# Kernel optimization log

Hardware: AMD Instinct MI355X
Metric: run time of the kernel (lower is better)

## Reference

```python
import jax, jax.numpy as jnp
import numpy as np

N_EMBED = 16384
EMBED_DIM = 256
BETA = 1.0  # default forward arg


def setup_inputs() -> dict:
    key = jax.random.key(0)
    k1, k2 = jax.random.split(key)
    z = jax.random.normal(k1, (8, EMBED_DIM, 32, 32), dtype=jnp.float32)
    # nn.Embedding init: uniform(-1/n_embed, 1/n_embed)
    embed_w = jax.random.uniform(k2, (N_EMBED, EMBED_DIM), dtype=jnp.float32,
                                 minval=-1.0 / N_EMBED, maxval=1.0 / N_EMBED)
    return {"z": z, "embed_w": embed_w}


def reference(z, embed_w):
    B, C, H, W = z.shape
    zb = jnp.transpose(z, (0, 2, 3, 1))            # (B,H,W,C)
    zf = zb.reshape(B * H * W, C)                  # (BHW, C)
    # squared L2 distances to every code: ||z||^2 + ||e||^2 - 2 z.e
    d = (jnp.sum(zf ** 2, axis=1, keepdims=True)
         + jnp.sum(embed_w ** 2, axis=1)
         - 2.0 * jnp.einsum('bd,nd->bn', zf, embed_w))  # (BHW, n_embed)
    idx = jnp.argmin(d, axis=1)                    # (BHW,)
    z_q = embed_w[idx].reshape(B, H, W, C)         # codebook gather
    loss = (BETA * jnp.mean((jax.lax.stop_gradient(z_q) - zb) ** 2)
            + jnp.mean((z_q - jax.lax.stop_gradient(zb)) ** 2))
    # straight-through estimator
    z_q = zb + jax.lax.stop_gradient(z_q - zb)
    z_q = jnp.transpose(z_q, (0, 3, 1, 2))         # (B,C,H,W)
    return z_q, loss
```

## Files before the change

kernel.cpp:

```cpp
#include <hip/hip_runtime.h>
#include <hip/hip_bf16.h>
#include <stdint.h>


typedef __attribute__((ext_vector_type(8))) short bf16x8;
typedef __attribute__((ext_vector_type(8))) unsigned short ushort8v;
typedef __attribute__((ext_vector_type(4))) float f32x4;

__device__ __forceinline__ unsigned short f2bf(float f) {
  unsigned u = __float_as_uint(f);
  return (unsigned short)((u + 0x7FFFu + ((u >> 16) & 1u)) >> 16);
}

typedef const __attribute__((address_space(1))) unsigned char* gas1;
typedef __attribute__((address_space(3))) unsigned char* las3;
__device__ __forceinline__ void cp16(const void* g, void* l) {
  __builtin_amdgcn_global_load_lds((gas1)g, (las3)l, 16, 0, 0);
}

__global__ void k_prep_z(const float* __restrict__ z, unsigned short* __restrict__ zp) {
  __shared__ float tile[32][129];
  int bid = blockIdx.x;
  int b = bid >> 6, ct = (bid >> 3) & 7, hwt = bid & 7;
  int t = threadIdx.x;
  const float* src = z + b * 262144 + ct * 32 * 1024 + hwt * 128;
#pragma unroll
  for (int it = 0; it < 16; ++it) {
    int e = it * 256 + t;
    int cl = e >> 7, hl = e & 127;
    tile[cl][hl] = src[cl * 1024 + hl];
  }
  __syncthreads();
  int mt = b * 8 + hwt;
  unsigned short* dst = zp + mt * 32768 + ct * 4096;
#pragma unroll
  for (int it = 0; it < 2; ++it) {
    int cell = it * 256 + t;
    int kg = cell >> 7, r = cell & 127;
    ushort8v v;
#pragma unroll
    for (int j = 0; j < 8; ++j) v[j] = f2bf(tile[kg * 8 + j][r]);
    *(ushort8v*)(dst + cell * 8) = v;
  }
}

__global__ void k_prep_e(const float* __restrict__ ew, unsigned short* __restrict__ ep,
                         float* __restrict__ h2) {
  int t = threadIdx.x;
  int n = blockIdx.x * 32 + (t >> 3);
  int nb = n >> 7, col = n & 127;
  float s = 0.0f;
#pragma unroll
  for (int it = 0; it < 4; ++it) {
    int cellk = (t & 7) + it * 8;
    const float4 x = *(const float4*)(ew + n * 256 + cellk * 8);
    const float4 y = *(const float4*)(ew + n * 256 + cellk * 8 + 4);
    s += x.x * x.x + x.y * x.y + x.z * x.z + x.w * x.w
       + y.x * y.x + y.y * y.y + y.z * y.z + y.w * y.w;
    int ks = cellk >> 2, kg = cellk & 3;
    ushort8v v;
    v[0] = f2bf(x.x); v[1] = f2bf(x.y); v[2] = f2bf(x.z); v[3] = f2bf(x.w);
    v[4] = f2bf(y.x); v[5] = f2bf(y.y); v[6] = f2bf(y.z); v[7] = f2bf(y.w);
    *(ushort8v*)(ep + nb * 32768 + ks * 4096 + kg * 1024 + col * 8) = v;
  }
#pragma unroll
  for (int off = 1; off <= 4; off <<= 1) s += __shfl_xor(s, off);
  if ((t & 7) == 0) h2[n] = 0.5f * s;
}

__global__ __launch_bounds__(256, 2) void k_main(
    const unsigned short* __restrict__ zp, const unsigned short* __restrict__ ep,
    const float* __restrict__ h2, int2* __restrict__ partial) {
  __shared__ unsigned char bLds[2][8192];
  int seg = blockIdx.x;
  int mt = blockIdx.y;
  int t = threadIdx.x, wv = t >> 6, lane = t & 63;
  int l15 = lane & 15, kg = lane >> 4;

  bf16x8 av[16];
  const unsigned short* abase = zp + mt * 32768;
#pragma unroll
  for (int m = 0; m < 2; ++m)
#pragma unroll
    for (int ks = 0; ks < 8; ++ks)
      av[m * 8 + ks] = *(const bf16x8*)(abase + ks * 4096 + kg * 1024 +
                                        (wv * 32 + m * 16 + l15) * 8);

  const unsigned char* bsrc = (const unsigned char*)ep + seg * 1048576;
  const float* hseg = h2 + seg * 2048;

#pragma unroll
  for (int i = 0; i < 2; ++i)
    cp16(bsrc + i * 4096 + wv * 1024 + lane * 16, &bLds[0][i * 4096 + wv * 1024]);

  float hv[8];
#pragma unroll
  for (int nf = 0; nf < 8; ++nf) hv[nf] = hseg[nf * 16 + l15];

  f32x4 acc[2][8];
#pragma unroll
  for (int m = 0; m < 2; ++m)
#pragma unroll
    for (int nf = 0; nf < 8; ++nf)
      acc[m][nf] = (f32x4){-hv[nf], -hv[nf], -hv[nf], -hv[nf]};

  float best[2][4];
#pragma unroll
  for (int m = 0; m < 2; ++m)
#pragma unroll
    for (int r = 0; r < 4; ++r) best[m][r] = -3.4e38f;

  __syncthreads();

  for (int ch = 0; ch < 16; ++ch) {
    float hn[8];
    if (ch < 15) {
#pragma unroll
      for (int nf = 0; nf < 8; ++nf) hn[nf] = hseg[(ch + 1) * 128 + nf * 16 + l15];
    }
#pragma unroll
    for (int ks = 0; ks < 8; ++ks) {
      int g = ch * 8 + ks;
      int cur = g & 1;
      if (g < 127) {
#pragma unroll
        for (int i = 0; i < 2; ++i)
          cp16(bsrc + (g + 1) * 8192 + i * 4096 + wv * 1024 + lane * 16,
               &bLds[cur ^ 1][i * 4096 + wv * 1024]);
      }
      bf16x8 bv[8];
#pragma unroll
      for (int nf = 0; nf < 8; ++nf)
        bv[nf] = *(const bf16x8*)(&bLds[cur][kg * 2048 + (nf * 16 + l15) * 16]);
#pragma unroll
      for (int m = 0; m < 2; ++m)
#pragma unroll
        for (int nf = 0; nf < 8; ++nf)
          acc[m][nf] = __builtin_amdgcn_mfma_f32_16x16x32_bf16(
              av[m * 8 + ks], bv[nf], acc[m][nf], 0, 0, 0);
      __syncthreads();
    }
    int colbase = ch * 128 + l15;
#pragma unroll
    for (int m = 0; m < 2; ++m)
#pragma unroll
      for (int nf = 0; nf < 8; ++nf) {
        unsigned lcol = (unsigned)(colbase + nf * 16);
#pragma unroll
        for (int r = 0; r < 4; ++r) {
          unsigned p = (__float_as_uint(acc[m][nf][r]) & 0xFFFFF800u) | lcol;
          best[m][r] = fmaxf(best[m][r], __uint_as_float(p));
        }
      }
    if (ch < 15) {
#pragma unroll
      for (int m = 0; m < 2; ++m)
#pragma unroll
        for (int nf = 0; nf < 8; ++nf)
          acc[m][nf] = (f32x4){-hn[nf], -hn[nf], -hn[nf], -hn[nf]};
    }
  }

#pragma unroll
  for (int m = 0; m < 2; ++m)
#pragma unroll
    for (int r = 0; r < 4; ++r) {
      float bvv = best[m][r];
#pragma unroll
      for (int off = 1; off <= 8; off <<= 1) bvv = fmaxf(bvv, __shfl_xor(bvv, off));
      if (l15 == 0) {
        unsigned bits = __float_as_uint(bvv);
        int gidx = seg * 2048 + (int)(bits & 0x7FFu);
        int row = mt * 128 + wv * 32 + m * 16 + kg * 4 + r;
        partial[seg * 8192 + row] = make_int2((int)bits, gidx);
      }
    }
}

__global__ void k_rg(const int2* __restrict__ partial, const float* __restrict__ ew,
                     float* __restrict__ rows) {
  int row = blockIdx.x * 4 + (threadIdx.x >> 6);
  int lane = threadIdx.x & 63;
  float bb = -3.4e38f;
  int bi = 0;
#pragma unroll
  for (int s = 0; s < 8; ++s) {
    int2 p = partial[s * 8192 + row];
    float v = __int_as_float(p.x);
    if (v > bb) { bb = v; bi = p.y; }
  }
  float4 v = *(const float4*)(ew + bi * 256 + lane * 4);
  *(float4*)(rows + row * 256 + lane * 4) = v;
}

__global__ void k_out(const float* __restrict__ rows, const float* __restrict__ z,
                      float* __restrict__ out) {
  __shared__ float tile[32][132];
  int bid = blockIdx.x;
  int b = bid >> 6, hwt = (bid >> 3) & 7, ct = bid & 7;
  int t = threadIdx.x;
  int hw0 = hwt * 128, c0 = ct * 32;
  const float* rbase = rows + (b * 1024 + hw0) * 256 + c0;
#pragma unroll
  for (int it = 0; it < 4; ++it) {
    int p = it * 32 + (t >> 3);
    int c = (t & 7) * 4;
    float4 v = *(const float4*)(rbase + p * 256 + c);
    tile[c][p] = v.x; tile[c + 1][p] = v.y; tile[c + 2][p] = v.z; tile[c + 3][p] = v.w;
  }
  __syncthreads();
  float ls = 0.0f;
  int obase = b * 262144 + c0 * 1024 + hw0;
#pragma unroll
  for (int it = 0; it < 4; ++it) {
    int c = it * 8 + (t >> 5);
    int p = (t & 31) * 4;
    float4 q = *(const float4*)(&tile[c][p]);
    float4 zv = *(const float4*)(z + obase + c * 1024 + p);
    float dx = q.x - zv.x, dy = q.y - zv.y, dz = q.z - zv.z, dw = q.w - zv.w;
    ls += dx * dx + dy * dy + dz * dz + dw * dw;
    *(float4*)(out + obase + c * 1024 + p) = q;
  }
#pragma unroll
  for (int off = 32; off; off >>= 1) ls += __shfl_xor(ls, off);
  if ((t & 63) == 0) atomicAdd(out + 2097152, ls * (2.0f / 2097152.0f));
}

extern "C" void kernel_launch(void* const* d_in, const int* in_sizes, int n_in,
                              void* d_out, int out_size, void* d_ws, size_t ws_size,
                              hipStream_t stream) {
  const float* z = (const float*)d_in[0];
  const float* ew = (const float*)d_in[1];
  float* out = (float*)d_out;
  unsigned char* ws = (unsigned char*)d_ws;
  unsigned short* zp = (unsigned short*)ws;
  unsigned short* ep = (unsigned short*)(ws + (4u << 20));
  float* h2 = (float*)(ws + (12u << 20));
  int2* partial = (int2*)(ws + (12u << 20) + 65536);
  float* rows = (float*)(ws + (13u << 20));

  k_prep_z<<<512, 256, 0, stream>>>(z, zp);
  k_prep_e<<<512, 256, 0, stream>>>(ew, ep, h2);
  k_main<<<dim3(8, 64), 256, 0, stream>>>(zp, ep, h2, partial);
  k_rg<<<2048, 256, 0, stream>>>(partial, ew, rows);
  hipMemsetAsync(out + 2097152, 0, 4, stream);
  k_out<<<512, 256, 0, stream>>>(rows, z, out);
}
```

Measured before the change: 180.7 us.

## Fuse prep and finalize kernels, double main grid segments, use larger k-stages

The z and codebook prep kernels are merged into one launch that also zeroes the loss slot, replacing the memset. The reduce-gather and output-transpose kernels are merged, so the intermediate gathered-rows buffer is no longer written and reread. The main kernel splits the codebook into 16 segments instead of 8 to launch more blocks, and stages 16KB of B per barrier instead of 8KB, halving the barrier count. It also raises launch bounds to 3 blocks per CU and wraps the MFMA section in s_setprio. In exchange, the finalize step reads twice as many partials and each main block uses more LDS.

```diff
diff --git a/kernel.cpp b/kernel.cpp
--- a/kernel.cpp
+++ b/kernel.cpp
@@ -18,60 +18,62 @@
   __builtin_amdgcn_global_load_lds((gas1)g, (las3)l, 16, 0, 0);
 }
 
-__global__ void k_prep_z(const float* __restrict__ z, unsigned short* __restrict__ zp) {
-  __shared__ float tile[32][129];
+__global__ void k_prep(const float* __restrict__ z, const float* __restrict__ ew,
+                       unsigned short* __restrict__ zp, unsigned short* __restrict__ ep,
+                       float* __restrict__ h2, float* __restrict__ out) {
+  __shared__ float tile[32][132];
   int bid = blockIdx.x;
-  int b = bid >> 6, ct = (bid >> 3) & 7, hwt = bid & 7;
   int t = threadIdx.x;
-  const float* src = z + b * 262144 + ct * 32 * 1024 + hwt * 128;
-#pragma unroll
-  for (int it = 0; it < 16; ++it) {
-    int e = it * 256 + t;
-    int cl = e >> 7, hl = e & 127;
-    tile[cl][hl] = src[cl * 1024 + hl];
-  }
-  __syncthreads();
-  int mt = b * 8 + hwt;
-  unsigned short* dst = zp + mt * 32768 + ct * 4096;
-#pragma unroll
-  for (int it = 0; it < 2; ++it) {
-    int cell = it * 256 + t;
-    int kg = cell >> 7, r = cell & 127;
-    ushort8v v;
-#pragma unroll
-    for (int j = 0; j < 8; ++j) v[j] = f2bf(tile[kg * 8 + j][r]);
-    *(ushort8v*)(dst + cell * 8) = v;
-  }
-}
-
-__global__ void k_prep_e(const float* __restrict__ ew, unsigned short* __restrict__ ep,
-                         float* __restrict__ h2) {
-  int t = threadIdx.x;
-  int n = blockIdx.x * 32 + (t >> 3);
-  int nb = n >> 7, col = n & 127;
-  float s = 0.0f;
-#pragma unroll
-  for (int it = 0; it < 4; ++it) {
-    int cellk = (t & 7) + it * 8;
-    const float4 x = *(const float4*)(ew + n * 256 + cellk * 8);
-    const float4 y = *(const float4*)(ew + n * 256 + cellk * 8 + 4);
-    s += x.x * x.x + x.y * x.y + x.z * x.z + x.w * x.w
-       + y.x * y.x + y.y * y.y + y.z * y.z + y.w * y.w;
-    int ks = cellk >> 2, kg = cellk & 3;
-    ushort8v v;
-    v[0] = f2bf(x.x); v[1] = f2bf(x.y); v[2] = f2bf(x.z); v[3] = f2bf(x.w);
-    v[4] = f2bf(y.x); v[5] = f2bf(y.y); v[6] = f2bf(y.z); v[7] = f2bf(y.w);
-    *(ushort8v*)(ep + nb * 32768 + ks * 4096 + kg * 1024 + col * 8) = v;
-  }
-#pragma unroll
-  for (int off = 1; off <= 4; off <<= 1) s += __shfl_xor(s, off);
-  if ((t & 7) == 0) h2[n] = 0.5f * s;
-}
-
-__global__ __launch_bounds__(256, 2) void k_main(
+  if (bid < 512) {
+    int b = bid >> 6, ct = (bid >> 3) & 7, hwt = bid & 7;
+    const float* src = z + b * 262144 + ct * 32768 + hwt * 128;
+#pragma unroll
+    for (int it = 0; it < 4; ++it) {
+      int cell = it * 1024 + t * 4;
+      int cl = cell >> 7, hl = cell & 127;
+      float4 v = *(const float4*)(src + cl * 1024 + hl);
+      *(float4*)(&tile[cl][hl]) = v;
+    }
+    __syncthreads();
+    int mt = b * 8 + hwt;
+    unsigned short* dst = zp + mt * 32768 + ct * 4096;
+#pragma unroll
+    for (int it = 0; it < 2; ++it) {
+      int cell = it * 256 + t;
+      int kg = cell >> 7, r = cell & 127;
+      ushort8v v;
+#pragma unroll
+      for (int j = 0; j < 8; ++j) v[j] = f2bf(tile[kg * 8 + j][r]);
+      *(ushort8v*)(dst + cell * 8) = v;
+    }
+  } else {
+    if (bid == 512 && t == 0) out[2097152] = 0.0f;
+    int n = (bid - 512) * 32 + (t >> 3);
+    int nb = n >> 7, col = n & 127;
+    float s = 0.0f;
+#pragma unroll
+    for (int it = 0; it < 4; ++it) {
+      int cellk = (t & 7) + it * 8;
+      const float4 x = *(const float4*)(ew + n * 256 + cellk * 8);
+      const float4 y = *(const float4*)(ew + n * 256 + cellk * 8 + 4);
+      s += x.x * x.x + x.y * x.y + x.z * x.z + x.w * x.w
+         + y.x * y.x + y.y * y.y + y.z * y.z + y.w * y.w;
+      int ks = cellk >> 2, kg = cellk & 3;
+      ushort8v v;
+      v[0] = f2bf(x.x); v[1] = f2bf(x.y); v[2] = f2bf(x.z); v[3] = f2bf(x.w);
+      v[4] = f2bf(y.x); v[5] = f2bf(y.y); v[6] = f2bf(y.z); v[7] = f2bf(y.w);
+      *(ushort8v*)(ep + nb * 32768 + ks * 4096 + kg * 1024 + col * 8) = v;
+    }
+#pragma unroll
+    for (int off = 1; off <= 4; off <<= 1) s += __shfl_xor(s, off);
+    if ((t & 7) == 0) h2[n] = 0.5f * s;
+  }
+}
+
+__global__ __launch_bounds__(256, 3) void k_main(
     const unsigned short* __restrict__ zp, const unsigned short* __restrict__ ep,
     const float* __restrict__ h2, int2* __restrict__ partial) {
-  __shared__ unsigned char bLds[2][8192];
+  __shared__ unsigned char bLds[2][16384];
   int seg = blockIdx.x;
   int mt = blockIdx.y;
   int t = threadIdx.x, wv = t >> 6, lane = t & 63;
@@ -86,79 +88,70 @@
       av[m * 8 + ks] = *(const bf16x8*)(abase + ks * 4096 + kg * 1024 +
                                         (wv * 32 + m * 16 + l15) * 8);
 
-  const unsigned char* bsrc = (const unsigned char*)ep + seg * 1048576;
-  const float* hseg = h2 + seg * 2048;
-
-#pragma unroll
-  for (int i = 0; i < 2; ++i)
+  const unsigned char* bsrc = (const unsigned char*)ep + seg * 524288;
+  const float* hseg = h2 + seg * 1024;
+
+#pragma unroll
+  for (int i = 0; i < 4; ++i)
     cp16(bsrc + i * 4096 + wv * 1024 + lane * 16, &bLds[0][i * 4096 + wv * 1024]);
 
-  float hv[8];
-#pragma unroll
-  for (int nf = 0; nf < 8; ++nf) hv[nf] = hseg[nf * 16 + l15];
-
   f32x4 acc[2][8];
+  float best[2][4];
 #pragma unroll
   for (int m = 0; m < 2; ++m)
 #pragma unroll
-    for (int nf = 0; nf < 8; ++nf)
-      acc[m][nf] = (f32x4){-hv[nf], -hv[nf], -hv[nf], -hv[nf]};
-
-  float best[2][4];
-#pragma unroll
-  for (int m = 0; m < 2; ++m)
-#pragma unroll
     for (int r = 0; r < 4; ++r) best[m][r] = -3.4e38f;
 
   __syncthreads();
 
-  for (int ch = 0; ch < 16; ++ch) {
-    float hn[8];
-    if (ch < 15) {
-#pragma unroll
-      for (int nf = 0; nf < 8; ++nf) hn[nf] = hseg[(ch + 1) * 128 + nf * 16 + l15];
-    }
-#pragma unroll
-    for (int ks = 0; ks < 8; ++ks) {
-      int g = ch * 8 + ks;
-      int cur = g & 1;
-      if (g < 127) {
-#pragma unroll
-        for (int i = 0; i < 2; ++i)
-          cp16(bsrc + (g + 1) * 8192 + i * 4096 + wv * 1024 + lane * 16,
-               &bLds[cur ^ 1][i * 4096 + wv * 1024]);
+#pragma unroll 4
+  for (int s = 0; s < 32; ++s) {
+    int cur = s & 1;
+    if (s < 31) {
+#pragma unroll
+      for (int i = 0; i < 4; ++i)
+        cp16(bsrc + (s + 1) * 16384 + i * 4096 + wv * 1024 + lane * 16,
+             &bLds[cur ^ 1][i * 4096 + wv * 1024]);
+    }
+    int nb = s >> 2, ph = s & 3;
+    if (ph == 0) {
+#pragma unroll
+      for (int nf = 0; nf < 8; ++nf) {
+        float h = hseg[nb * 128 + nf * 16 + l15];
+        acc[0][nf] = (f32x4){-h, -h, -h, -h};
+        acc[1][nf] = acc[0][nf];
       }
+    }
+    __builtin_amdgcn_s_setprio(1);
+#pragma unroll
+    for (int k2 = 0; k2 < 2; ++k2) {
       bf16x8 bv[8];
 #pragma unroll
       for (int nf = 0; nf < 8; ++nf)
-        bv[nf] = *(const bf16x8*)(&bLds[cur][kg * 2048 + (nf * 16 + l15) * 16]);
+        bv[nf] = *(const bf16x8*)(&bLds[cur][k2 * 8192 + kg * 2048 + (nf * 16 + l15) * 16]);
 #pragma unroll
       for (int m = 0; m < 2; ++m)
 #pragma unroll
         for (int nf = 0; nf < 8; ++nf)
           acc[m][nf] = __builtin_amdgcn_mfma_f32_16x16x32_bf16(
-              av[m * 8 + ks], bv[nf], acc[m][nf], 0, 0, 0);
-      __syncthreads();
-    }
-    int colbase = ch * 128 + l15;
-#pragma unroll
-    for (int m = 0; m < 2; ++m)
-#pragma unroll
-      for (int nf = 0; nf < 8; ++nf) {
-        unsigned lcol = (unsigned)(colbase + nf * 16);
-#pragma unroll
-        for (int r = 0; r < 4; ++r) {
-          unsigned p = (__float_as_uint(acc[m][nf][r]) & 0xFFFFF800u) | lcol;
-          best[m][r] = fmaxf(best[m][r], __uint_as_float(p));
+              av[m * 8 + ph * 2 + k2], bv[nf], acc[m][nf], 0, 0, 0);
+    }
+    __builtin_amdgcn_s_setprio(0);
+    if (ph == 3) {
+      int colbase = nb * 128 + l15;
+#pragma unroll
+      for (int m = 0; m < 2; ++m)
+#pragma unroll
+        for (int nf = 0; nf < 8; ++nf) {
+          unsigned lcol = (unsigned)(colbase + nf * 16);
+#pragma unroll
+          for (int r = 0; r < 4; ++r) {
+            unsigned p = (__float_as_uint(acc[m][nf][r]) & 0xFFFFF800u) | lcol;
+            best[m][r] = fmaxf(best[m][r], __uint_as_float(p));
+          }
         }
-      }
-    if (ch < 15) {
-#pragma unroll
-      for (int m = 0; m < 2; ++m)
-#pragma unroll
-        for (int nf = 0; nf < 8; ++nf)
-          acc[m][nf] = (f32x4){-hn[nf], -hn[nf], -hn[nf], -hn[nf]};
-    }
+    }
+    __syncthreads();
   }
 
 #pragma unroll
@@ -170,47 +163,48 @@
       for (int off = 1; off <= 8; off <<= 1) bvv = fmaxf(bvv, __shfl_xor(bvv, off));
       if (l15 == 0) {
         unsigned bits = __float_as_uint(bvv);
-        int gidx = seg * 2048 + (int)(bits & 0x7FFu);
+        int gidx = seg * 1024 + (int)(bits & 0x7FFu);
         int row = mt * 128 + wv * 32 + m * 16 + kg * 4 + r;
         partial[seg * 8192 + row] = make_int2((int)bits, gidx);
       }
     }
 }
 
-__global__ void k_rg(const int2* __restrict__ partial, const float* __restrict__ ew,
-                     float* __restrict__ rows) {
-  int row = blockIdx.x * 4 + (threadIdx.x >> 6);
-  int lane = threadIdx.x & 63;
-  float bb = -3.4e38f;
-  int bi = 0;
-#pragma unroll
-  for (int s = 0; s < 8; ++s) {
-    int2 p = partial[s * 8192 + row];
-    float v = __int_as_float(p.x);
-    if (v > bb) { bb = v; bi = p.y; }
-  }
-  float4 v = *(const float4*)(ew + bi * 256 + lane * 4);
-  *(float4*)(rows + row * 256 + lane * 4) = v;
-}
-
-__global__ void k_out(const float* __restrict__ rows, const float* __restrict__ z,
-                      float* __restrict__ out) {
+__global__ void k_fin(const int2* __restrict__ partial, const float* __restrict__ ew,
+                      const float* __restrict__ z, float* __restrict__ out) {
   __shared__ float tile[32][132];
+  __shared__ int codeIdx[128];
   int bid = blockIdx.x;
   int b = bid >> 6, hwt = (bid >> 3) & 7, ct = bid & 7;
   int t = threadIdx.x;
-  int hw0 = hwt * 128, c0 = ct * 32;
-  const float* rbase = rows + (b * 1024 + hw0) * 256 + c0;
-#pragma unroll
-  for (int it = 0; it < 4; ++it) {
-    int p = it * 32 + (t >> 3);
-    int c = (t & 7) * 4;
-    float4 v = *(const float4*)(rbase + p * 256 + c);
-    tile[c][p] = v.x; tile[c + 1][p] = v.y; tile[c + 2][p] = v.z; tile[c + 3][p] = v.w;
+  int rowbase = b * 1024 + hwt * 128;
+  if (t < 128) {
+    int row = rowbase + t;
+    float bb = -3.4e38f;
+    int bi = 0;
+#pragma unroll
+    for (int s = 0; s < 16; ++s) {
+      int2 p = partial[s * 8192 + row];
+      float v = __int_as_float(p.x);
+      if (v > bb) { bb = v; bi = p.y; }
+    }
+    codeIdx[t] = bi;
+  }
+  __syncthreads();
+  int c0 = ct * 32;
+  {
+    int p = t >> 1, half = t & 1;
+    const float* er = ew + codeIdx[p] * 256 + c0 + half * 16;
+#pragma unroll
+    for (int j = 0; j < 4; ++j) {
+      float4 v = *(const float4*)(er + j * 4);
+      int c = half * 16 + j * 4;
+      tile[c][p] = v.x; tile[c + 1][p] = v.y; tile[c + 2][p] = v.z; tile[c + 3][p] = v.w;
+    }
   }
   __syncthreads();
   float ls = 0.0f;
-  int obase = b * 262144 + c0 * 1024 + hw0;
+  int obase = b * 262144 + c0 * 1024 + hwt * 128;
 #pragma unroll
   for (int it = 0; it < 4; ++it) {
     int c = it * 8 + (t >> 5);
@@ -237,12 +231,8 @@
   unsigned short* ep = (unsigned short*)(ws + (4u << 20));
   float* h2 = (float*)(ws + (12u << 20));
   int2* partial = (int2*)(ws + (12u << 20) + 65536);
-  float* rows = (float*)(ws + (13u << 20));
-
-  k_prep_z<<<512, 256, 0, stream>>>(z, zp);
-  k_prep_e<<<512, 256, 0, stream>>>(ew, ep, h2);
-  k_main<<<dim3(8, 64), 256, 0, stream>>>(zp, ep, h2, partial);
-  k_rg<<<2048, 256, 0, stream>>>(partial, ew, rows);
-  hipMemsetAsync(out + 2097152, 0, 4, stream);
-  k_out<<<512, 256, 0, stream>>>(rows, z, out);
-}
+
+  k_prep<<<1024, 256, 0, stream>>>(z, ew, zp, ep, h2, out);
+  k_main<<<dim3(16, 64), 256, 0, stream>>>(zp, ep, h2, partial);
+  k_fin<<<512, 256, 0, stream>>>(partial, ew, z, out);
+}
```

Result: faster. 176.4 us (-2.4%).
